# Performance work log

Measured on AMD Instinct MI355X. Metric: run time of the kernel, lower is better.

Reference implementation:

```python
import jax, jax.numpy as jnp
import numpy as np

S, B, D, Z, C, H = 256, 1024, 64, 32, 64, 128
L = 2 * S + 3  # len(ext_ts); _xs[0::2][1:-1] must match xs -> L = 2*S+3


def setup_inputs() -> dict:
    key = jax.random.key(0)
    ks = jax.random.split(key, 16)

    def xavier(k, out_d, in_d):
        lim = float(np.sqrt(6.0 / (in_d + out_d)))
        return jax.random.uniform(k, (out_d, in_d), minval=-lim, maxval=lim, dtype=jnp.float32)

    bias = lambda n: jnp.full((n,), 0.01, jnp.float32)  # m.bias.data.fill_(0.01)

    return {
        "xs": jax.random.normal(ks[0], (S, B, D), jnp.float32),
        "ext_ts": jnp.arange(L, dtype=jnp.float32) * 0.01,  # spacing <= dt=0.02 -> 1 euler step/interval
        "eps_z0": jax.random.normal(ks[1], (B, Z), jnp.float32),
        "dW": jax.random.normal(ks[2], (L - 1, B, Z), jnp.float32),  # standard normal; scaled by sqrt(dt) inside
        "gru_Wih": xavier(ks[3], 3 * H, D),
        "gru_Whh": xavier(ks[4], 3 * H, H),
        "gru_bih": jnp.zeros((3 * H,), jnp.float32),
        "gru_bhh": jnp.zeros((3 * H,), jnp.float32),
        "enc_W": xavier(ks[5], C, H), "enc_b": bias(C),
        "qz0_W": xavier(ks[6], 2 * Z, C), "qz0_b": bias(2 * Z),
        "f_W1": xavier(ks[7], H, Z + 1), "f_b1": bias(H),
        "f_W2": xavier(ks[8], H, H), "f_b2": bias(H),
        "f_W3": xavier(ks[9], Z, H), "f_b3": bias(Z),
        "g_W1": xavier(ks[10], H, Z + 1), "g_b1": bias(H),
        "g_W2": xavier(ks[11], Z, H), "g_b2": bias(Z),
        "proj_W": xavier(ks[12], D, Z), "proj_b": bias(D),
        "pz0_mean": jnp.zeros((1, Z), jnp.float32),
        "pz0_logstd": jnp.zeros((1, Z), jnp.float32),
    }


def reference(xs, ext_ts, eps_z0, dW, gru_Wih, gru_Whh, gru_bih, gru_bhh,
              enc_W, enc_b, qz0_W, qz0_b,
              f_W1, f_b1, f_W2, f_b2, f_W3, f_b3,
              g_W1, g_b1, g_W2, g_b2,
              proj_W, proj_b, pz0_mean, pz0_logstd):
    nb = xs.shape[1]
    # ---- Encoder: GRU over time-reversed xs; only ctx[0] (after flip-back) is
    # used, which equals lin(final hidden of the reversed-sequence GRU).
    x_rev = xs[::-1]
    gi_all = jnp.einsum('sbd,hd->sbh', x_rev, gru_Wih) + gru_bih  # (S,B,3H)

    def gru_step(h, gi_t):
        gh = h @ gru_Whh.T + gru_bhh
        i_r, i_z, i_n = jnp.split(gi_t, 3, axis=-1)
        h_r, h_z, h_n = jnp.split(gh, 3, axis=-1)
        r = jax.nn.sigmoid(i_r + h_r)
        zg = jax.nn.sigmoid(i_z + h_z)
        n = jnp.tanh(i_n + r * h_n)
        return (1.0 - zg) * n + zg * h, None

    hT, _ = jax.lax.scan(gru_step, jnp.zeros((nb, gru_Whh.shape[1]), xs.dtype), gi_all)
    ctx0 = hT @ enc_W.T + enc_b

    # ---- q(z0) and reparameterized sample
    q = ctx0 @ qz0_W.T + qz0_b
    qz0_mean, qz0_logstd = jnp.split(q, 2, axis=1)
    z0 = qz0_mean + jnp.exp(qz0_logstd) * eps_z0

    # ---- Euler-Maruyama SDE integration (diagonal noise), one step per interval
    dts = ext_ts[1:] - ext_ts[:-1]

    def sde_step(z, inp):
        t, dt, dw = inp
        tcol = jnp.broadcast_to(t.reshape(1, 1), (z.shape[0], 1)).astype(z.dtype)
        tz = jnp.concatenate([tcol, z], axis=1)  # (B, Z+1)
        h1 = jax.nn.relu(tz @ f_W1.T + f_b1)
        h2 = jax.nn.relu(h1 @ f_W2.T + f_b2)
        drift = h2 @ f_W3.T + f_b3
        gh = jax.nn.relu(tz @ g_W1.T + g_b1)
        diff = gh @ g_W2.T + g_b2
        z_new = z + drift * dt + diff * (jnp.sqrt(dt) * dw)
        return z_new, z_new

    _, zs_rest = jax.lax.scan(sde_step, z0, (ext_ts[:-1], dts, dW))
    zs = jnp.concatenate([z0[None], zs_rest], axis=0)  # (L,B,Z)

    # ---- project to data space and compute losses
    xs_hat = jnp.einsum('lbz,dz->lbd', zs, proj_W) + proj_b
    recon_xs = xs_hat[0::2][1:-1]   # (S,B,D)
    interp_xs = xs_hat[1::2][1:-1]  # (S-1,B,D)
    recon_loss = jnp.mean((recon_xs - xs) ** 2)

    # KL( N(qm, e^qls) || N(pm, e^pls) ), summed over latent, averaged over batch
    kl = (pz0_logstd - qz0_logstd
          + (jnp.exp(2.0 * qz0_logstd) + (qz0_mean - pz0_mean) ** 2)
          / (2.0 * jnp.exp(2.0 * pz0_logstd)) - 0.5)
    logqp0 = jnp.mean(jnp.sum(kl, axis=1))
    return recon_loss, logqp0, interp_xs
```

## Files before the change

### kernel.cpp

```cpp
#include <hip/hip_runtime.h>

typedef _Float16 f16;
typedef _Float16 h2 __attribute__((ext_vector_type(2)));
typedef _Float16 h8 __attribute__((ext_vector_type(8)));
typedef _Float16 v8h __attribute__((ext_vector_type(8)));
typedef _Float16 v4h __attribute__((ext_vector_type(4)));
typedef float    f4 __attribute__((ext_vector_type(4)));
typedef float    v4f __attribute__((ext_vector_type(4)));
typedef float    f2 __attribute__((ext_vector_type(2)));

#define S_  256
#define B_  1024
#define D_  64
#define H_  128
#define Z_  32
#define BD_ (B_*D_)
#define NSTEP 514

__device__ __forceinline__ h8 ld8(const float* p) {
  f4 a = *(const f4*)p;
  f4 b = *(const f4*)(p + 4);
  h8 w;
  w[0]=(f16)a[0]; w[1]=(f16)a[1]; w[2]=(f16)a[2]; w[3]=(f16)a[3];
  w[4]=(f16)b[0]; w[5]=(f16)b[1]; w[6]=(f16)b[2]; w[7]=(f16)b[3];
  return w;
}

__device__ __forceinline__ float sigm(float x) { return 1.f / (1.f + __expf(-x)); }
__device__ __forceinline__ float tanh_(float x) {
  float e = __expf(-2.f * fabsf(x));
  float t = (1.f - e) / (1.f + e);
  return copysignf(t, x);
}

__global__ __launch_bounds__(256, 1) void gru_mfma_kernel(
    const float* __restrict__ xs, const float* __restrict__ Wih,
    const float* __restrict__ Whh, const float* __restrict__ bih,
    const float* __restrict__ bhh, float* __restrict__ hT)
{
  __shared__ f16 hB[2][16][136];

  const int t    = threadIdx.x;
  const int wid  = t >> 6;
  const int lane = t & 63;
  const int lr = lane & 15;
  const int lg = lane >> 4;
  const int r0 = blockIdx.x * 16;

  v8h whhR[2][4], whhZ[2][4], whhN[2][4];
  v8h wihR[2][2], wihZ[2][2], wihN[2][2];
  #pragma unroll
  for (int tt = 0; tt < 2; ++tt) {
    const int nr = wid*32 + tt*16 + lr;
    #pragma unroll
    for (int ks = 0; ks < 4; ++ks) {
      whhR[tt][ks] = ld8(Whh + (      nr)*H_ + ks*32 + lg*8);
      whhZ[tt][ks] = ld8(Whh + (128 + nr)*H_ + ks*32 + lg*8);
      whhN[tt][ks] = ld8(Whh + (256 + nr)*H_ + ks*32 + lg*8);
    }
    #pragma unroll
    for (int ks = 0; ks < 2; ++ks) {
      wihR[tt][ks] = ld8(Wih + (      nr)*D_ + ks*32 + lg*8);
      wihZ[tt][ks] = ld8(Wih + (128 + nr)*D_ + ks*32 + lg*8);
      wihN[tt][ks] = ld8(Wih + (256 + nr)*D_ + ks*32 + lg*8);
    }
  }
  v4f birh[2], bizh[2], binv[2], bhnv[2];
  #pragma unroll
  for (int tt = 0; tt < 2; ++tt) {
    const int nb = wid*32 + tt*16 + lg*4;
    v4f a = *(const v4f*)&bih[nb],     b = *(const v4f*)&bhh[nb];
    v4f c = *(const v4f*)&bih[128+nb], d = *(const v4f*)&bhh[128+nb];
    birh[tt] = a + b;
    bizh[tt] = c + d;
    binv[tt] = *(const v4f*)&bih[256+nb];
    bhnv[tt] = *(const v4f*)&bhh[256+nb];
  }

  for (int i = t; i < 16*136; i += 256) ((f16*)hB[0])[i] = (f16)0.f;
  v4f hm[2] = { {0.f,0.f,0.f,0.f}, {0.f,0.f,0.f,0.f} };
  const v4f zero4 = {0.f, 0.f, 0.f, 0.f};

  v8h bx0 = ld8(xs + (S_-1)*BD_ + (r0+lr)*D_ + lg*8);
  v8h bx1 = ld8(xs + (S_-1)*BD_ + (r0+lr)*D_ + 32 + lg*8);
  __syncthreads();

  int p = 0;
  #pragma unroll 1
  for (int s = 0; s < S_; ++s) {
    v8h nx0 = bx0, nx1 = bx1;
    if (s < S_-1) {
      const float* xp = xs + (S_-2-s)*BD_ + (r0+lr)*D_;
      nx0 = ld8(xp + lg*8);
      nx1 = ld8(xp + 32 + lg*8);
    }
    v8h bh[4];
    #pragma unroll
    for (int ks = 0; ks < 4; ++ks)
      bh[ks] = *(const v8h*)&hB[p][lr][ks*32 + lg*8];

    #pragma unroll
    for (int tt = 0; tt < 2; ++tt) {
      v4f ar  = __builtin_amdgcn_mfma_f32_16x16x32_f16(wihR[tt][0], bx0, zero4, 0,0,0);
      v4f az  = __builtin_amdgcn_mfma_f32_16x16x32_f16(wihZ[tt][0], bx0, zero4, 0,0,0);
      v4f anx = __builtin_amdgcn_mfma_f32_16x16x32_f16(wihN[tt][0], bx0, zero4, 0,0,0);
      ar  = __builtin_amdgcn_mfma_f32_16x16x32_f16(wihR[tt][1], bx1, ar,  0,0,0);
      az  = __builtin_amdgcn_mfma_f32_16x16x32_f16(wihZ[tt][1], bx1, az,  0,0,0);
      anx = __builtin_amdgcn_mfma_f32_16x16x32_f16(wihN[tt][1], bx1, anx, 0,0,0);
      v4f anh = zero4;
      #pragma unroll
      for (int ks = 0; ks < 4; ++ks) {
        ar  = __builtin_amdgcn_mfma_f32_16x16x32_f16(whhR[tt][ks], bh[ks], ar,  0,0,0);
        az  = __builtin_amdgcn_mfma_f32_16x16x32_f16(whhZ[tt][ks], bh[ks], az,  0,0,0);
        anh = __builtin_amdgcn_mfma_f32_16x16x32_f16(whhN[tt][ks], bh[ks], anh, 0,0,0);
      }
      v4h o;
      #pragma unroll
      for (int i = 0; i < 4; ++i) {
        float r  = sigm(ar[i] + birh[tt][i]);
        float zg = sigm(az[i] + bizh[tt][i]);
        float n  = tanh_(anx[i] + binv[tt][i] + r*(anh[i] + bhnv[tt][i]));
        hm[tt][i] = (1.f - zg)*n + zg*hm[tt][i];
        o[i] = (f16)hm[tt][i];
      }
      *(v4h*)&hB[p^1][lr][wid*32 + tt*16 + lg*4] = o;
    }
    __syncthreads();
    p ^= 1;
    bx0 = nx0; bx1 = nx1;
  }

  #pragma unroll
  for (int tt = 0; tt < 2; ++tt)
    *(v4f*)&hT[(r0+lr)*H_ + wid*32 + tt*16 + lg*4] = hm[tt];
}

__global__ __launch_bounds__(256) void enc_kernel(
    const float* __restrict__ hT, const float* __restrict__ encW,
    const float* __restrict__ encB, const float* __restrict__ qW,
    const float* __restrict__ qB, const float* __restrict__ eps,
    const float* __restrict__ pm, const float* __restrict__ pls,
    float* __restrict__ z0, float* __restrict__ out)
{
  __shared__ float hTl[4][128];
  __shared__ float ctx[4][64];
  __shared__ float ql[4][64];
  const int t = threadIdx.x;
  const int b0 = blockIdx.x * 4;
  const int lb = t >> 6, j = t & 63;

  for (int i = t; i < 512; i += 256) hTl[i>>7][i&127] = hT[b0*H_ + i];
  __syncthreads();

  float acc = encB[j];
  #pragma unroll
  for (int k = 0; k < 128; k += 4) {
    f4 w = *(const f4*)&encW[j*128 + k];
    acc += hTl[lb][k]*w[0] + hTl[lb][k+1]*w[1] + hTl[lb][k+2]*w[2] + hTl[lb][k+3]*w[3];
  }
  ctx[lb][j] = acc;
  __syncthreads();

  float q = qB[j];
  #pragma unroll
  for (int k = 0; k < 64; k += 4) {
    f4 w = *(const f4*)&qW[j*64 + k];
    q += ctx[lb][k]*w[0] + ctx[lb][k+1]*w[1] + ctx[lb][k+2]*w[2] + ctx[lb][k+3]*w[3];
  }
  ql[lb][j] = q;
  __syncthreads();

  float kl = 0.f;
  if (j < 32) {
    float mean = ql[lb][j], ls = ql[lb][j+32];
    z0[(b0+lb)*Z_ + j] = mean + __expf(ls)*eps[(b0+lb)*Z_ + j];
    float pmj = pm[j], plsj = pls[j];
    float dm = mean - pmj;
    kl = plsj - ls + (__expf(2.f*ls) + dm*dm) / (2.f*__expf(2.f*plsj)) - 0.5f;
  }
  #pragma unroll
  for (int s2 = 32; s2 > 0; s2 >>= 1) kl += __shfl_down(kl, s2, 64);
  if (j == 0) atomicAdd(out + 1, kl * (1.f/1024.f));
}

__global__ __launch_bounds__(256, 1) void sde_mfma_kernel(
    const float* __restrict__ z0, const float* __restrict__ ts,
    const float* __restrict__ dW, const float* __restrict__ xs,
    const float* __restrict__ fW1, const float* __restrict__ fb1,
    const float* __restrict__ fW2, const float* __restrict__ fb2,
    const float* __restrict__ fW3, const float* __restrict__ fb3,
    const float* __restrict__ gW1, const float* __restrict__ gb1,
    const float* __restrict__ gW2, const float* __restrict__ gb2,
    const float* __restrict__ pW, const float* __restrict__ pb,
    float* __restrict__ out)
{
  __shared__ f16 Xa[16*72];
  __shared__ f16 h1A[16*168];
  __shared__ f16 ghA[16*168];
  __shared__ f16 h2A[16*168];
  __shared__ float tsL[516];
  __shared__ float lred[4];

  const int t    = threadIdx.x;
  const int wid  = t >> 6;
  const int lane = t & 63;
  const int lr = lane & 15;
  const int lg = lane >> 4;
  const int r0 = blockIdx.x * 16;
  const int wz = wid & 1;

  v8h w1r[8];
  #pragma unroll
  for (int nl = 0; nl < 4; ++nl) {
    const int n = wid*4 + nl;
    const float* src = (n < 8) ? (fW1 + (n*16+lr)*33) : (gW1 + ((n-8)*16+lr)*33);
    const float bsv  = (n < 8) ? fb1[n*16+lr] : gb1[(n-8)*16+lr];
    #pragma unroll
    for (int ks = 0; ks < 2; ++ks) {
      v8h w;
      #pragma unroll
      for (int j = 0; j < 8; ++j) {
        const int kp = ks*32 + lg*8 + j;
        float v;
        if (kp < 32)                   v = src[1+kp];
        else if (kp == 32 || kp == 34) v = src[0];
        else if (kp == 33)             v = bsv;
        else                           v = 0.f;
        w[j] = (f16)v;
      }
      w1r[nl*2+ks] = w;
    }
  }
  v8h w2r[10];
  #pragma unroll
  for (int nl = 0; nl < 2; ++nl) {
    const int n = wid*2 + nl;
    const float* src = fW2 + (n*16+lr)*128;
    const float bsv = fb2[n*16+lr];
    #pragma unroll
    for (int ks = 0; ks < 5; ++ks) {
      v8h w;
      #pragma unroll
      for (int j = 0; j < 8; ++j) {
        const int kp = ks*32 + lg*8 + j;
        float v = (kp < 128) ? src[kp] : ((kp == 128) ? bsv : 0.f);
        w[j] = (f16)v;
      }
      w2r[nl*5+ks] = w;
    }
  }
  v8h w3d[5], w3g[5];
  {
    const float* sd = fW3 + (wz*16+lr)*128;
    const float* sg = gW2 + (wz*16+lr)*128;
    const float bd = fb3[wz*16+lr], bg = gb2[wz*16+lr];
    #pragma unroll
    for (int ks = 0; ks < 5; ++ks) {
      v8h wd, wg;
      #pragma unroll
      for (int j = 0; j < 8; ++j) {
        const int kp = ks*32 + lg*8 + j;
        wd[j] = (f16)((kp < 128) ? sd[kp] : ((kp == 128) ? bd : 0.f));
        wg[j] = (f16)((kp < 128) ? sg[kp] : ((kp == 128) ? bg : 0.f));
      }
      w3d[ks] = wd; w3g[ks] = wg;
    }
  }
  v8h pwr[2];
  {
    const float* sp = pW + (wid*16+lr)*32;
    const float bp = pb[wid*16+lr];
    #pragma unroll
    for (int ks = 0; ks < 2; ++ks) {
      v8h w;
      #pragma unroll
      for (int j = 0; j < 8; ++j) {
        const int kp = ks*32 + lg*8 + j;
        w[j] = (f16)((kp < 32) ? sp[kp] : ((kp == 33) ? bp : 0.f));
      }
      pwr[ks] = w;
    }
  }

  for (int i = t; i < 16*72; i += 256) Xa[i] = (f16)0.f;
  for (int i = t; i < 16*168; i += 256) {
    h1A[i] = (f16)0.f; ghA[i] = (f16)0.f; h2A[i] = (f16)0.f;
  }
  for (int i = t; i < 515; i += 256) tsL[i] = ts[i];
  __syncthreads();
  if (t < 16) {
    Xa[t*72 + 33] = (f16)1.f;
    h1A[t*168 + 128] = (f16)1.f;
    ghA[t*168 + 128] = (f16)1.f;
    h2A[t*168 + 128] = (f16)1.f;
    const float t0 = tsL[0];
    const f16 th = (f16)t0;
    Xa[t*72 + 32] = th;
    Xa[t*72 + 34] = (f16)(t0 - (float)th);
  }
  const v4f zero4 = {0.f, 0.f, 0.f, 0.f};
  v4f zm = zero4;
  if (wid < 2) {
    zm = *(const v4f*)&z0[(r0+lr)*Z_ + wid*16 + lg*4];
    v4h a;
    #pragma unroll
    for (int i = 0; i < 4; ++i) a[i] = (f16)zm[i];
    *(v4h*)&Xa[lr*72 + wid*16 + lg*4] = a;
  }
  float loss = 0.f;
  __syncthreads();

  #pragma unroll 1
  for (int l = 0; l < NSTEP; ++l) {
    const float dt  = tsL[l+1] - tsL[l];
    const float sdt = sqrtf(dt);
    const int ln = l + 1;
    const bool ev = ((ln & 1) == 0) && ln >= 2 && ln <= 512;
    const bool od = ((ln & 1) == 1) && ln >= 3 && ln <= 511;

    v4f dwv = zero4;
    if (wid < 2) dwv = *(const v4f*)&dW[(l*B_ + r0 + lr)*Z_ + wid*16 + lg*4];
    v4f xv = zero4;
    if (ev) xv = *(const v4f*)&xs[(((ln-2)>>1)*B_ + r0 + lr)*D_ + wid*16 + lg*4];

    {
      const v8h bx0 = *(const v8h*)&Xa[lr*72 +  0 + lg*8];
      const v8h bx1 = *(const v8h*)&Xa[lr*72 + 32 + lg*8];
      #pragma unroll
      for (int nl = 0; nl < 4; ++nl) {
        v4f acc = __builtin_amdgcn_mfma_f32_16x16x32_f16(w1r[nl*2+0], bx0, zero4, 0, 0, 0);
        acc = __builtin_amdgcn_mfma_f32_16x16x32_f16(w1r[nl*2+1], bx1, acc, 0, 0, 0);
        v4h o;
        #pragma unroll
        for (int i = 0; i < 4; ++i) o[i] = (f16)fmaxf(acc[i], 0.f);
        if (wid < 2) *(v4h*)&h1A[lr*168 + (wid*4+nl)*16 + lg*4] = o;
        else         *(v4h*)&ghA[lr*168 + ((wid-2)*4+nl)*16 + lg*4] = o;
      }
    }
    __syncthreads();

    {
      v8h bh[5];
      #pragma unroll
      for (int ks = 0; ks < 5; ++ks) bh[ks] = *(const v8h*)&h1A[lr*168 + ks*32 + lg*8];
      #pragma unroll
      for (int nl = 0; nl < 2; ++nl) {
        v4f acc = zero4;
        #pragma unroll
        for (int ks = 0; ks < 5; ++ks)
          acc = __builtin_amdgcn_mfma_f32_16x16x32_f16(w2r[nl*5+ks], bh[ks], acc, 0, 0, 0);
        v4h o;
        #pragma unroll
        for (int i = 0; i < 4; ++i) o[i] = (f16)fmaxf(acc[i], 0.f);
        *(v4h*)&h2A[lr*168 + (wid*2+nl)*16 + lg*4] = o;
      }
    }
    __syncthreads();

    if (wid < 2) {
      v4f dac = zero4, fac = zero4;
      #pragma unroll
      for (int ks = 0; ks < 5; ++ks) {
        const v8h b2f = *(const v8h*)&h2A[lr*168 + ks*32 + lg*8];
        const v8h bgf = *(const v8h*)&ghA[lr*168 + ks*32 + lg*8];
        dac = __builtin_amdgcn_mfma_f32_16x16x32_f16(w3d[ks], b2f, dac, 0, 0, 0);
        fac = __builtin_amdgcn_mfma_f32_16x16x32_f16(w3g[ks], bgf, fac, 0, 0, 0);
      }
      #pragma unroll
      for (int i = 0; i < 4; ++i) zm[i] += dac[i]*dt + fac[i]*(sdt*dwv[i]);
      v4h a;
      #pragma unroll
      for (int i = 0; i < 4; ++i) a[i] = (f16)zm[i];
      *(v4h*)&Xa[lr*72 + wid*16 + lg*4] = a;
    } else if (wid == 3 && lg == 0) {
      const float tn = tsL[l+1];
      const f16 th = (f16)tn;
      Xa[lr*72 + 32] = th;
      Xa[lr*72 + 34] = (f16)(tn - (float)th);
    }
    __syncthreads();

    if (ev || od) {
      const v8h px0 = *(const v8h*)&Xa[lr*72 +  0 + lg*8];
      const v8h px1 = *(const v8h*)&Xa[lr*72 + 32 + lg*8];
      v4f a = __builtin_amdgcn_mfma_f32_16x16x32_f16(pwr[0], px0, zero4, 0, 0, 0);
      v4f p = __builtin_amdgcn_mfma_f32_16x16x32_f16(pwr[1], px1, a, 0, 0, 0);
      if (ev) {
        #pragma unroll
        for (int i = 0; i < 4; ++i) { float d = p[i] - xv[i]; loss = fmaf(d, d, loss); }
      } else {
        float* op = out + 2 + (((ln-3)>>1)*B_ + r0 + lr)*D_ + wid*16 + lg*4;
        *(f2*)&op[0] = (f2){p[0], p[1]};
        *(f2*)&op[2] = (f2){p[2], p[3]};
      }
    }
  }

  #pragma unroll
  for (int s2 = 32; s2 > 0; s2 >>= 1) loss += __shfl_down(loss, s2, 64);
  if (lane == 0) lred[wid] = loss;
  __syncthreads();
  if (t == 0)
    atomicAdd(out + 0, (lred[0] + lred[1] + lred[2] + lred[3]) * (1.f/16777216.f));
}

extern "C" void kernel_launch(void* const* d_in, const int* in_sizes, int n_in,
                              void* d_out, int out_size, void* d_ws, size_t ws_size,
                              hipStream_t stream) {
  (void)in_sizes; (void)n_in; (void)out_size; (void)ws_size;
  const float* xs   = (const float*)d_in[0];
  const float* ts   = (const float*)d_in[1];
  const float* eps  = (const float*)d_in[2];
  const float* dWp  = (const float*)d_in[3];
  const float* Wih  = (const float*)d_in[4];
  const float* Whh  = (const float*)d_in[5];
  const float* bih  = (const float*)d_in[6];
  const float* bhh  = (const float*)d_in[7];
  const float* encW = (const float*)d_in[8];
  const float* encB = (const float*)d_in[9];
  const float* qW   = (const float*)d_in[10];
  const float* qB   = (const float*)d_in[11];
  const float* fW1  = (const float*)d_in[12];
  const float* fb1  = (const float*)d_in[13];
  const float* fW2  = (const float*)d_in[14];
  const float* fb2  = (const float*)d_in[15];
  const float* fW3  = (const float*)d_in[16];
  const float* fb3  = (const float*)d_in[17];
  const float* gW1  = (const float*)d_in[18];
  const float* gb1  = (const float*)d_in[19];
  const float* gW2  = (const float*)d_in[20];
  const float* gb2  = (const float*)d_in[21];
  const float* pW   = (const float*)d_in[22];
  const float* pb   = (const float*)d_in[23];
  const float* pm   = (const float*)d_in[24];
  const float* pls  = (const float*)d_in[25];

  float* out = (float*)d_out;
  float* ws  = (float*)d_ws;
  float* hT = ws;
  float* z0 = ws + 131072;

  hipMemsetAsync(d_out, 0, 2*sizeof(float), stream);
  hipLaunchKernelGGL(gru_mfma_kernel, dim3(64), dim3(256), 0, stream,
                     xs, Wih, Whh, bih, bhh, hT);
  hipLaunchKernelGGL(enc_kernel, dim3(256), dim3(256), 0, stream,
                     hT, encW, encB, qW, qB, eps, pm, pls, z0, out);
  hipLaunchKernelGGL(sde_mfma_kernel, dim3(64), dim3(256), 0, stream,
                     z0, ts, dWp, xs, fW1, fb1, fW2, fb2, fW3, fb3,
                     gW1, gb1, gW2, gb2, pW, pb, out);
}
```

Baseline: 1.270 ms.

## Widen GRU blocks to 8 waves, rebalance SDE wave work, prefetch per-step inputs

The GRU kernel now runs 512 threads per block, so each of 8 waves owns one 16-column output tile instead of two. This halves the serial MFMA chain per wave on the recurrent critical path. In the SDE kernel, waves 2-3 now compute the diffusion output layer concurrently with the second drift layer and pass it through shared memory. Layer-2 tiles are redistributed 3/3/1/1 across the waves, and the dW and xs loads are prefetched one step ahead. The cost is more barrier participants in the GRU kernel, an extra LDS buffer, and uneven wave workloads in the SDE kernel.

```diff
diff --git a/kernel.cpp b/kernel.cpp
--- a/kernel.cpp
+++ b/kernel.cpp
@@ -33,7 +33,7 @@
   return copysignf(t, x);
 }
 
-__global__ __launch_bounds__(256, 1) void gru_mfma_kernel(
+__global__ __launch_bounds__(512, 1) void gru_mfma_kernel(
     const float* __restrict__ xs, const float* __restrict__ Wih,
     const float* __restrict__ Whh, const float* __restrict__ bih,
     const float* __restrict__ bhh, float* __restrict__ hT)
@@ -47,38 +47,28 @@
   const int lg = lane >> 4;
   const int r0 = blockIdx.x * 16;
 
-  v8h whhR[2][4], whhZ[2][4], whhN[2][4];
-  v8h wihR[2][2], wihZ[2][2], wihN[2][2];
-  #pragma unroll
-  for (int tt = 0; tt < 2; ++tt) {
-    const int nr = wid*32 + tt*16 + lr;
-    #pragma unroll
-    for (int ks = 0; ks < 4; ++ks) {
-      whhR[tt][ks] = ld8(Whh + (      nr)*H_ + ks*32 + lg*8);
-      whhZ[tt][ks] = ld8(Whh + (128 + nr)*H_ + ks*32 + lg*8);
-      whhN[tt][ks] = ld8(Whh + (256 + nr)*H_ + ks*32 + lg*8);
-    }
-    #pragma unroll
-    for (int ks = 0; ks < 2; ++ks) {
-      wihR[tt][ks] = ld8(Wih + (      nr)*D_ + ks*32 + lg*8);
-      wihZ[tt][ks] = ld8(Wih + (128 + nr)*D_ + ks*32 + lg*8);
-      wihN[tt][ks] = ld8(Wih + (256 + nr)*D_ + ks*32 + lg*8);
-    }
-  }
-  v4f birh[2], bizh[2], binv[2], bhnv[2];
-  #pragma unroll
-  for (int tt = 0; tt < 2; ++tt) {
-    const int nb = wid*32 + tt*16 + lg*4;
-    v4f a = *(const v4f*)&bih[nb],     b = *(const v4f*)&bhh[nb];
-    v4f c = *(const v4f*)&bih[128+nb], d = *(const v4f*)&bhh[128+nb];
-    birh[tt] = a + b;
-    bizh[tt] = c + d;
-    binv[tt] = *(const v4f*)&bih[256+nb];
-    bhnv[tt] = *(const v4f*)&bhh[256+nb];
-  }
-
-  for (int i = t; i < 16*136; i += 256) ((f16*)hB[0])[i] = (f16)0.f;
-  v4f hm[2] = { {0.f,0.f,0.f,0.f}, {0.f,0.f,0.f,0.f} };
+  const int nr = wid*16 + lr;
+  v8h whR[4], whZ[4], whN[4], wiR[2], wiZ[2], wiN[2];
+  #pragma unroll
+  for (int ks = 0; ks < 4; ++ks) {
+    whR[ks] = ld8(Whh + (      nr)*H_ + ks*32 + lg*8);
+    whZ[ks] = ld8(Whh + (128 + nr)*H_ + ks*32 + lg*8);
+    whN[ks] = ld8(Whh + (256 + nr)*H_ + ks*32 + lg*8);
+  }
+  #pragma unroll
+  for (int ks = 0; ks < 2; ++ks) {
+    wiR[ks] = ld8(Wih + (      nr)*D_ + ks*32 + lg*8);
+    wiZ[ks] = ld8(Wih + (128 + nr)*D_ + ks*32 + lg*8);
+    wiN[ks] = ld8(Wih + (256 + nr)*D_ + ks*32 + lg*8);
+  }
+  const int nb = wid*16 + lg*4;
+  const v4f birh = *(const v4f*)&bih[nb]     + *(const v4f*)&bhh[nb];
+  const v4f bizh = *(const v4f*)&bih[128+nb] + *(const v4f*)&bhh[128+nb];
+  const v4f binv = *(const v4f*)&bih[256+nb];
+  const v4f bhnv = *(const v4f*)&bhh[256+nb];
+
+  for (int i = t; i < 16*136; i += 512) ((f16*)hB[0])[i] = (f16)0.f;
+  v4f hm = {0.f, 0.f, 0.f, 0.f};
   const v4f zero4 = {0.f, 0.f, 0.f, 0.f};
 
   v8h bx0 = ld8(xs + (S_-1)*BD_ + (r0+lr)*D_ + lg*8);
@@ -99,40 +89,35 @@
     for (int ks = 0; ks < 4; ++ks)
       bh[ks] = *(const v8h*)&hB[p][lr][ks*32 + lg*8];
 
-    #pragma unroll
-    for (int tt = 0; tt < 2; ++tt) {
-      v4f ar  = __builtin_amdgcn_mfma_f32_16x16x32_f16(wihR[tt][0], bx0, zero4, 0,0,0);
-      v4f az  = __builtin_amdgcn_mfma_f32_16x16x32_f16(wihZ[tt][0], bx0, zero4, 0,0,0);
-      v4f anx = __builtin_amdgcn_mfma_f32_16x16x32_f16(wihN[tt][0], bx0, zero4, 0,0,0);
-      ar  = __builtin_amdgcn_mfma_f32_16x16x32_f16(wihR[tt][1], bx1, ar,  0,0,0);
-      az  = __builtin_amdgcn_mfma_f32_16x16x32_f16(wihZ[tt][1], bx1, az,  0,0,0);
-      anx = __builtin_amdgcn_mfma_f32_16x16x32_f16(wihN[tt][1], bx1, anx, 0,0,0);
-      v4f anh = zero4;
-      #pragma unroll
-      for (int ks = 0; ks < 4; ++ks) {
-        ar  = __builtin_amdgcn_mfma_f32_16x16x32_f16(whhR[tt][ks], bh[ks], ar,  0,0,0);
-        az  = __builtin_amdgcn_mfma_f32_16x16x32_f16(whhZ[tt][ks], bh[ks], az,  0,0,0);
-        anh = __builtin_amdgcn_mfma_f32_16x16x32_f16(whhN[tt][ks], bh[ks], anh, 0,0,0);
-      }
-      v4h o;
-      #pragma unroll
-      for (int i = 0; i < 4; ++i) {
-        float r  = sigm(ar[i] + birh[tt][i]);
-        float zg = sigm(az[i] + bizh[tt][i]);
-        float n  = tanh_(anx[i] + binv[tt][i] + r*(anh[i] + bhnv[tt][i]));
-        hm[tt][i] = (1.f - zg)*n + zg*hm[tt][i];
-        o[i] = (f16)hm[tt][i];
-      }
-      *(v4h*)&hB[p^1][lr][wid*32 + tt*16 + lg*4] = o;
-    }
+    v4f ar  = __builtin_amdgcn_mfma_f32_16x16x32_f16(wiR[0], bx0, zero4, 0,0,0);
+    v4f az  = __builtin_amdgcn_mfma_f32_16x16x32_f16(wiZ[0], bx0, zero4, 0,0,0);
+    v4f anx = __builtin_amdgcn_mfma_f32_16x16x32_f16(wiN[0], bx0, zero4, 0,0,0);
+    ar  = __builtin_amdgcn_mfma_f32_16x16x32_f16(wiR[1], bx1, ar,  0,0,0);
+    az  = __builtin_amdgcn_mfma_f32_16x16x32_f16(wiZ[1], bx1, az,  0,0,0);
+    anx = __builtin_amdgcn_mfma_f32_16x16x32_f16(wiN[1], bx1, anx, 0,0,0);
+    v4f anh = zero4;
+    #pragma unroll
+    for (int ks = 0; ks < 4; ++ks) {
+      ar  = __builtin_amdgcn_mfma_f32_16x16x32_f16(whR[ks], bh[ks], ar,  0,0,0);
+      az  = __builtin_amdgcn_mfma_f32_16x16x32_f16(whZ[ks], bh[ks], az,  0,0,0);
+      anh = __builtin_amdgcn_mfma_f32_16x16x32_f16(whN[ks], bh[ks], anh, 0,0,0);
+    }
+    v4h o;
+    #pragma unroll
+    for (int i = 0; i < 4; ++i) {
+      float r  = sigm(ar[i] + birh[i]);
+      float zg = sigm(az[i] + bizh[i]);
+      float n  = tanh_(anx[i] + binv[i] + r*(anh[i] + bhnv[i]));
+      hm[i] = (1.f - zg)*n + zg*hm[i];
+      o[i] = (f16)hm[i];
+    }
+    *(v4h*)&hB[p^1][lr][wid*16 + lg*4] = o;
     __syncthreads();
     p ^= 1;
     bx0 = nx0; bx1 = nx1;
   }
 
-  #pragma unroll
-  for (int tt = 0; tt < 2; ++tt)
-    *(v4f*)&hT[(r0+lr)*H_ + wid*32 + tt*16 + lg*4] = hm[tt];
+  *(v4f*)&hT[(r0+lr)*H_ + wid*16 + lg*4] = hm;
 }
 
 __global__ __launch_bounds__(256) void enc_kernel(
@@ -198,6 +183,7 @@
   __shared__ f16 h1A[16*168];
   __shared__ f16 ghA[16*168];
   __shared__ f16 h2A[16*168];
+  __shared__ float diffL[16][36];
   __shared__ float tsL[516];
   __shared__ float lred[4];
 
@@ -207,7 +193,6 @@
   const int lr = lane & 15;
   const int lg = lane >> 4;
   const int r0 = blockIdx.x * 16;
-  const int wz = wid & 1;
 
   v8h w1r[8];
   #pragma unroll
@@ -231,39 +216,42 @@
       w1r[nl*2+ks] = w;
     }
   }
-  v8h w2r[10];
-  #pragma unroll
-  for (int nl = 0; nl < 2; ++nl) {
-    const int n = wid*2 + nl;
-    const float* src = fW2 + (n*16+lr)*128;
-    const float bsv = fb2[n*16+lr];
+  const int nt2 = (wid < 2) ? 3 : 1;
+  const int tb2 = (wid < 2) ? wid*3 : 6 + (wid - 2);
+  v8h w2r[15];
+  #pragma unroll
+  for (int nl = 0; nl < 3; ++nl) {
+    if (nl < nt2) {
+      const int n = tb2 + nl;
+      const float* src = fW2 + (n*16+lr)*128;
+      const float bsv = fb2[n*16+lr];
+      #pragma unroll
+      for (int ks = 0; ks < 5; ++ks) {
+        v8h w;
+        #pragma unroll
+        for (int j = 0; j < 8; ++j) {
+          const int kp = ks*32 + lg*8 + j;
+          float v = (kp < 128) ? src[kp] : ((kp == 128) ? bsv : 0.f);
+          w[j] = (f16)v;
+        }
+        w2r[nl*5+ks] = w;
+      }
+    }
+  }
+  v8h w3[5];
+  {
+    const int zh = (wid < 2) ? wid : (wid - 2);
+    const float* s3 = (wid < 2) ? (fW3 + (zh*16+lr)*128) : (gW2 + (zh*16+lr)*128);
+    const float b3 = (wid < 2) ? fb3[zh*16+lr] : gb2[zh*16+lr];
     #pragma unroll
     for (int ks = 0; ks < 5; ++ks) {
       v8h w;
       #pragma unroll
       for (int j = 0; j < 8; ++j) {
         const int kp = ks*32 + lg*8 + j;
-        float v = (kp < 128) ? src[kp] : ((kp == 128) ? bsv : 0.f);
-        w[j] = (f16)v;
-      }
-      w2r[nl*5+ks] = w;
-    }
-  }
-  v8h w3d[5], w3g[5];
-  {
-    const float* sd = fW3 + (wz*16+lr)*128;
-    const float* sg = gW2 + (wz*16+lr)*128;
-    const float bd = fb3[wz*16+lr], bg = gb2[wz*16+lr];
-    #pragma unroll
-    for (int ks = 0; ks < 5; ++ks) {
-      v8h wd, wg;
-      #pragma unroll
-      for (int j = 0; j < 8; ++j) {
-        const int kp = ks*32 + lg*8 + j;
-        wd[j] = (f16)((kp < 128) ? sd[kp] : ((kp == 128) ? bd : 0.f));
-        wg[j] = (f16)((kp < 128) ? sg[kp] : ((kp == 128) ? bg : 0.f));
-      }
-      w3d[ks] = wd; w3g[ks] = wg;
+        w[j] = (f16)((kp < 128) ? s3[kp] : ((kp == 128) ? b3 : 0.f));
+      }
+      w3[ks] = w;
     }
   }
   v8h pwr[2];
@@ -308,6 +296,8 @@
     *(v4h*)&Xa[lr*72 + wid*16 + lg*4] = a;
   }
   float loss = 0.f;
+  v4f dwv = zero4, xv = zero4;
+  if (wid < 2) dwv = *(const v4f*)&dW[(0*B_ + r0 + lr)*Z_ + wid*16 + lg*4];
   __syncthreads();
 
   #pragma unroll 1
@@ -318,10 +308,14 @@
     const bool ev = ((ln & 1) == 0) && ln >= 2 && ln <= 512;
     const bool od = ((ln & 1) == 1) && ln >= 3 && ln <= 511;
 
-    v4f dwv = zero4;
-    if (wid < 2) dwv = *(const v4f*)&dW[(l*B_ + r0 + lr)*Z_ + wid*16 + lg*4];
-    v4f xv = zero4;
-    if (ev) xv = *(const v4f*)&xs[(((ln-2)>>1)*B_ + r0 + lr)*D_ + wid*16 + lg*4];
+    v4f dwN = zero4, xvN = zero4;
+    if (wid < 2 && l + 1 < NSTEP)
+      dwN = *(const v4f*)&dW[((l+1)*B_ + r0 + lr)*Z_ + wid*16 + lg*4];
+    {
+      const int ln2 = l + 2;
+      if (((ln2 & 1) == 0) && ln2 >= 2 && ln2 <= 512)
+        xvN = *(const v4f*)&xs[(((ln2-2)>>1)*B_ + r0 + lr)*D_ + wid*16 + lg*4];
+    }
 
     {
       const v8h bx0 = *(const v8h*)&Xa[lr*72 +  0 + lg*8];
@@ -340,34 +334,44 @@
     __syncthreads();
 
     {
+      if (wid >= 2) {
+        v4f fac = zero4;
+        #pragma unroll
+        for (int ks = 0; ks < 5; ++ks) {
+          const v8h bgf = *(const v8h*)&ghA[lr*168 + ks*32 + lg*8];
+          fac = __builtin_amdgcn_mfma_f32_16x16x32_f16(w3[ks], bgf, fac, 0, 0, 0);
+        }
+        *(v4f*)&diffL[lr][(wid-2)*16 + lg*4] = fac;
+      }
       v8h bh[5];
       #pragma unroll
       for (int ks = 0; ks < 5; ++ks) bh[ks] = *(const v8h*)&h1A[lr*168 + ks*32 + lg*8];
       #pragma unroll
-      for (int nl = 0; nl < 2; ++nl) {
-        v4f acc = zero4;
-        #pragma unroll
-        for (int ks = 0; ks < 5; ++ks)
-          acc = __builtin_amdgcn_mfma_f32_16x16x32_f16(w2r[nl*5+ks], bh[ks], acc, 0, 0, 0);
-        v4h o;
-        #pragma unroll
-        for (int i = 0; i < 4; ++i) o[i] = (f16)fmaxf(acc[i], 0.f);
-        *(v4h*)&h2A[lr*168 + (wid*2+nl)*16 + lg*4] = o;
+      for (int nl = 0; nl < 3; ++nl) {
+        if (nl < nt2) {
+          v4f acc = zero4;
+          #pragma unroll
+          for (int ks = 0; ks < 5; ++ks)
+            acc = __builtin_amdgcn_mfma_f32_16x16x32_f16(w2r[nl*5+ks], bh[ks], acc, 0, 0, 0);
+          v4h o;
+          #pragma unroll
+          for (int i = 0; i < 4; ++i) o[i] = (f16)fmaxf(acc[i], 0.f);
+          *(v4h*)&h2A[lr*168 + (tb2+nl)*16 + lg*4] = o;
+        }
       }
     }
     __syncthreads();
 
     if (wid < 2) {
-      v4f dac = zero4, fac = zero4;
+      v4f dac = zero4;
       #pragma unroll
       for (int ks = 0; ks < 5; ++ks) {
         const v8h b2f = *(const v8h*)&h2A[lr*168 + ks*32 + lg*8];
-        const v8h bgf = *(const v8h*)&ghA[lr*168 + ks*32 + lg*8];
-        dac = __builtin_amdgcn_mfma_f32_16x16x32_f16(w3d[ks], b2f, dac, 0, 0, 0);
-        fac = __builtin_amdgcn_mfma_f32_16x16x32_f16(w3g[ks], bgf, fac, 0, 0, 0);
-      }
-      #pragma unroll
-      for (int i = 0; i < 4; ++i) zm[i] += dac[i]*dt + fac[i]*(sdt*dwv[i]);
+        dac = __builtin_amdgcn_mfma_f32_16x16x32_f16(w3[ks], b2f, dac, 0, 0, 0);
+      }
+      const v4f dv = *(const v4f*)&diffL[lr][wid*16 + lg*4];
+      #pragma unroll
+      for (int i = 0; i < 4; ++i) zm[i] += dac[i]*dt + dv[i]*(sdt*dwv[i]);
       v4h a;
       #pragma unroll
       for (int i = 0; i < 4; ++i) a[i] = (f16)zm[i];
@@ -394,6 +398,7 @@
         *(f2*)&op[2] = (f2){p[2], p[3]};
       }
     }
+    dwv = dwN; xv = xvN;
   }
 
   #pragma unroll
@@ -441,7 +446,7 @@
   float* z0 = ws + 131072;
 
   hipMemsetAsync(d_out, 0, 2*sizeof(float), stream);
-  hipLaunchKernelGGL(gru_mfma_kernel, dim3(64), dim3(256), 0, stream,
+  hipLaunchKernelGGL(gru_mfma_kernel, dim3(64), dim3(512), 0, stream,
                      xs, Wih, Whh, bih, bhh, hT);
   hipLaunchKernelGGL(enc_kernel, dim3(256), dim3(256), 0, stream,
                      hT, encW, encB, qW, qB, eps, pm, pls, z0, out);
```

Result: slower. 1.325 ms (+4.3%).
